# Kernel optimization log

Hardware: AMD Instinct MI355X
Metric: run time of the kernel (lower is better)

The kernel has to match this reference:

```python
import jax, jax.numpy as jnp
import numpy as np

CH = 64          # channels per plane
GS = 256         # base grid size
N_PTS = 500_000  # query points
BOUND = 1.0
A = -0.75        # torch bicubic coefficient


def _avg_pool(p):
    # torch F.avg_pool2d(kernel=3, stride=2, padding=1, count_include_pad=True) on (C,H,W)
    s = jax.lax.reduce_window(p, 0.0, jax.lax.add, (1, 3, 3), (1, 2, 2),
                              [(0, 0), (1, 1), (1, 1)])
    return s / 9.0


def _cubic_w(t):
    # Keys cubic conv weights (a=-0.75) for taps at offsets [-1,0,1,2]; t in [0,1). -> (4, M)
    def k1(x):  # |x| <= 1
        return ((A + 2.0) * x - (A + 3.0)) * x * x + 1.0
    def k2(x):  # 1 < |x| < 2
        return ((A * x - 5.0 * A) * x + 8.0 * A) * x - 4.0 * A
    return jnp.stack([k2(t + 1.0), k1(t), k1(1.0 - t), k2(2.0 - t)])


def _sample_plane(plane, gx, gy):
    # bicubic grid_sample, padding_mode='border', align_corners=True
    # plane: (C,H,W); gx,gy: (M,) grid coords in [-1,1] convention. -> (M,C)
    C, H, W = plane.shape
    x = (gx + 1.0) * 0.5 * (W - 1)  # unnormalize (align_corners=True)
    y = (gy + 1.0) * 0.5 * (H - 1)
    x0 = jnp.floor(x)
    y0 = jnp.floor(y)
    wx = _cubic_w(x - x0)  # (4,M)
    wy = _cubic_w(y - y0)  # (4,M)
    offs = jnp.arange(-1, 3, dtype=jnp.int32)[:, None]
    ix = jnp.clip(x0.astype(jnp.int32)[None, :] + offs, 0, W - 1)  # (4,M) border clamp
    iy = jnp.clip(y0.astype(jnp.int32)[None, :] + offs, 0, H - 1)
    out = jnp.zeros((C, x.shape[0]), plane.dtype)
    for j in range(4):
        row = wx[0] * plane[:, iy[j], ix[0]]
        for i in range(1, 4):
            row = row + wx[i] * plane[:, iy[j], ix[i]]  # (C,M) gather + fma
        out = out + wy[j] * row
    return out.T  # (M,C)


def setup_inputs() -> dict:
    key = jax.random.key(0)
    kc, kx, ky, kz = jax.random.split(key, 4)
    coordinates = jax.random.uniform(kc, (N_PTS, 3), jnp.float32, -1.0, 1.0)
    px0 = jax.random.normal(kx, (CH, GS, GS), jnp.float32) * 0.001
    py0 = jax.random.normal(ky, (CH, GS, GS), jnp.float32) * 0.001
    pz0 = jax.random.normal(kz, (CH, GS, GS), jnp.float32) * 0.001
    px1, py1, pz1 = _avg_pool(px0), _avg_pool(py0), _avg_pool(pz0)
    px2, py2, pz2 = _avg_pool(px1), _avg_pool(py1), _avg_pool(pz1)
    return dict(coordinates=coordinates, px0=px0, py0=py0, pz0=pz0,
                px1=px1, py1=py1, pz1=pz1, px2=px2, py2=py2, pz2=pz2)


def reference(coordinates, px0, py0, pz0, px1, py1, pz1, px2, py2, pz2):
    # Faithful to torch: coords mapped to [0,1] and fed to grid_sample as-is
    c = (coordinates + BOUND) / (2.0 * BOUND)  # (N,3), lives in [0,1] of the [-1,1] grid space
    feats = []
    for pxy, pyz, pxz in ((px0, py0, pz0), (px1, py1, pz1), (px2, py2, pz2)):
        f = (_sample_plane(pxy, c[:, 0], c[:, 1])
             + _sample_plane(pyz, c[:, 1], c[:, 2])
             + _sample_plane(pxz, c[:, 0], c[:, 2]))
        feats.append(f)
    return jnp.concatenate(feats, axis=-1)  # (N, 3*CH)
```

## Files before the change

### kernel.cpp

```cpp
#include <hip/hip_runtime.h>
#include <hip/hip_fp16.h>

#define NPTS 500000
#define NBINS 32768
#define NSUPER 8192
#define RSTRIDE 65

#define PLANE_SCALE 1024.0f
#define INV_PLANE_SCALE 0.0009765625f

__device__ __forceinline__ void cubic_w(float t, float w[4]) {
  const float a = -0.75f;
  const float t1 = t + 1.0f;
  w[0] = ((a * t1 - 5.0f * a) * t1 + 8.0f * a) * t1 - 4.0f * a;
  w[1] = ((a + 2.0f) * t - (a + 3.0f)) * t * t + 1.0f;
  const float u = 1.0f - t;
  w[2] = ((a + 2.0f) * u - (a + 3.0f)) * u * u + 1.0f;
  const float t2 = 2.0f - t;
  w[3] = ((a * t2 - 5.0f * a) * t2 + 8.0f * a) * t2 - 4.0f * a;
}

__global__ __launch_bounds__(256) void transpose_chw_hwc_f16(
    const float* __restrict__ p0, const float* __restrict__ p1,
    const float* __restrict__ p2, __half* __restrict__ dst, int HW) {
  __shared__ float lds[64][65];
  const float* src = (blockIdx.y == 0) ? p0 : ((blockIdx.y == 1) ? p1 : p2);
  __half* out = dst + (size_t)blockIdx.y * (size_t)HW * 64;
  const int pixBase = blockIdx.x * 64;
  const int tid = threadIdx.x;
  const int lane = tid & 63;
  const int quad = tid >> 6;
#pragma unroll
  for (int k = 0; k < 16; ++k) {
    const int c = k * 4 + quad;
    lds[c][lane] = src[(size_t)c * HW + pixBase + lane];
  }
  __syncthreads();
#pragma unroll
  for (int k = 0; k < 16; ++k) {
    const int pp = k * 4 + quad;
    out[(size_t)(pixBase + pp) * 64 + lane] =
        __float2half(lds[lane][pp] * PLANE_SCALE);
  }
}

__device__ __forceinline__ unsigned spread3(unsigned v) {
  return (v & 1u) | ((v & 2u) << 2) | ((v & 4u) << 4) | ((v & 8u) << 6) |
         ((v & 16u) << 8);
}

__device__ __forceinline__ unsigned compact3(unsigned v) {
  return (v & 1u) | ((v >> 2) & 2u) | ((v >> 4) & 4u) | ((v >> 6) & 8u) |
         ((v >> 8) & 16u);
}

__device__ __forceinline__ int bin_of(float cx, float cy, float cz) {
  int xq = (int)((cx + 1.0f) * 16.0f);
  int yq = (int)((cy + 1.0f) * 16.0f);
  int zq = (int)((cz + 1.0f) * 16.0f);
  xq = xq < 0 ? 0 : (xq > 31 ? 31 : xq);
  yq = yq < 0 ? 0 : (yq > 31 ? 31 : yq);
  zq = zq < 0 ? 0 : (zq > 31 ? 31 : zq);
  return (int)(spread3((unsigned)xq) | (spread3((unsigned)yq) << 1) |
               (spread3((unsigned)zq) << 2));
}

__global__ __launch_bounds__(256) void bin_count(
    const float* __restrict__ coords, int* __restrict__ counts) {
  const int pt = blockIdx.x * 256 + threadIdx.x;
  if (pt >= NPTS) return;
  const int b = bin_of(coords[pt * 3], coords[pt * 3 + 1], coords[pt * 3 + 2]);
  atomicAdd(&counts[b], 1);
}

__global__ __launch_bounds__(1024) void bin_scan(
    const int* __restrict__ counts, int* __restrict__ cursor) {
  __shared__ int lds[1024];
  const int t = threadIdx.x;
  const int base = t * 32;
  int s = 0;
#pragma unroll
  for (int i = 0; i < 32; ++i) s += counts[base + i];
  lds[t] = s;
  __syncthreads();
  int own = s;
  for (int off = 1; off < 1024; off <<= 1) {
    int v = (t >= off) ? lds[t - off] : 0;
    __syncthreads();
    lds[t] += v;
    __syncthreads();
  }
  int run = lds[t] - own;
#pragma unroll
  for (int i = 0; i < 32; ++i) {
    cursor[base + i] = run;
    run += counts[base + i];
  }
}

__global__ __launch_bounds__(256) void bin_scatter_prep(
    const float* __restrict__ coords, int* __restrict__ cursor,
    uint4* __restrict__ wrec) {
  const int pt = blockIdx.x * 256 + threadIdx.x;
  if (pt >= NPTS) return;
  const float x = coords[pt * 3], y = coords[pt * 3 + 1],
              z = coords[pt * 3 + 2];
  const int b = bin_of(x, y, z);
  const int pos = atomicAdd(&cursor[b], 1);

  const int qx0 = ((int)compact3((unsigned)b)) & ~1;
  const int qy0 = ((int)compact3((unsigned)b >> 1)) & ~1;
  const int qz = (int)compact3((unsigned)b >> 2);
  const float vin[3] = {x, y, z};

#pragma unroll
  for (int s = 0; s < 3; ++s) {
    const int W = (s == 0) ? 256 : ((s == 1) ? 128 : 64);
    const float hw = 0.5f * (float)(W - 1);
    const int fb[3] = {(int)floorf((1.0f + (float)qx0 * 0.03125f) * hw),
                       (int)floorf((1.0f + (float)qy0 * 0.03125f) * hw),
                       (int)floorf((1.0f + (float)qz * 0.03125f) * hw)};
    uint wp[6];
    int rel[3];
#pragma unroll
    for (int a = 0; a < 3; ++a) {
      const float c = (vin[a] + 1.0f) * 0.5f;
      const float gx = (c + 1.0f) * 0.5f * (float)(W - 1);
      const float x0f = floorf(gx);
      float w[4];
      cubic_w(gx - x0f, w);
      int r = (int)x0f - fb[a];
      const int rmax = (a == 2) ? 4 : 12;
      r = r < 0 ? 0 : (r > rmax ? rmax : r);
      rel[a] = r;
      const __half2 lo = __halves2half2(__float2half(w[0]), __float2half(w[1]));
      const __half2 hi = __halves2half2(__float2half(w[2]), __float2half(w[3]));
      wp[a * 2] = *(const uint*)&lo;
      wp[a * 2 + 1] = *(const uint*)&hi;
    }
    uint4* dst = wrec + ((size_t)s * NPTS + pos) * 2;
    dst[0] = make_uint4(wp[0], wp[1], wp[2], wp[3]);
    dst[1] = make_uint4(
        wp[4], wp[5],
        (uint)(rel[0] * 4) | ((uint)(rel[1] * 4) << 8) | ((uint)rel[2] << 16),
        (uint)pt);
  }
}

__global__ __launch_bounds__(256, 4) void sample_super(
    const uint4* __restrict__ wrec, const ushort* __restrict__ tp,
    const int* __restrict__ endc, float* __restrict__ out) {
  __shared__ uint4 win[32 * RSTRIDE];

  const int orig = blockIdx.x;
  const int sb = (orig & 7) * (NSUPER / 8) + (orig >> 3);
  const int b0 = sb * 4;
  const int start = (b0 == 0) ? 0 : endc[b0 - 1];
  const int end = endc[b0 + 3];
  if (start >= end) return;

  const int s = blockIdx.y;
  const int h = blockIdx.z;
  const int W = (s == 0) ? 256 : ((s == 1) ? 128 : 64);
  const size_t sbase = (s == 0) ? 0 : ((s == 1) ? 12582912 : 15728640);
  const size_t psz = (size_t)W * W * 64;
  const float hw = 0.5f * (float)(W - 1);

  const int qx0 = ((int)compact3((unsigned)b0)) & ~1;
  const int qy0 = ((int)compact3((unsigned)b0 >> 1)) & ~1;
  const int qz = (int)compact3((unsigned)b0 >> 2);
  const int wbx = (int)floorf((1.0f + (float)qx0 * 0.03125f) * hw) - 1;
  const int wby = (int)floorf((1.0f + (float)qy0 * 0.03125f) * hw) - 1;
  const int wbz = (int)floorf((1.0f + (float)qz * 0.03125f) * hw) - 1;

  const char* tpb = (const char*)(tp + sbase) + h * 64;
  const int tid = threadIdx.x;
  const int wave = tid >> 6;
  const int lane = tid & 63;
  const int px = lane >> 2;
  const int cgl = lane & 3;
#pragma unroll
  for (int k = 0; k < 8; ++k) {
    const int row = k * 4 + wave;
    int p, grow, cb;
    if (row < 16) {
      p = 0;
      grow = wby + row;
      cb = wbx;
    } else if (row < 24) {
      p = 1;
      grow = wbz + row - 16;
      cb = wby;
    } else {
      p = 2;
      grow = wbz + row - 24;
      cb = wbx;
    }
    grow = grow < 0 ? 0 : (grow > W - 1 ? W - 1 : grow);
    int gcol = cb + px;
    gcol = gcol < 0 ? 0 : (gcol > W - 1 ? W - 1 : gcol);
    const char* src = tpb + (size_t)p * psz * 2 +
                      ((size_t)grow * W + gcol) * 128 + cgl * 16;
#if __has_builtin(__builtin_amdgcn_global_load_lds)
    __builtin_amdgcn_global_load_lds((const uint*)src,
                                     (uint*)&win[row * RSTRIDE], 16, 0, 0);
#else
    win[row * RSTRIDE + lane] = *reinterpret_cast<const uint4*>(src);
#endif
  }
  __syncthreads();

  const int lanegrp = tid >> 2;
  const int cg = tid & 3;

  for (int i0 = start; i0 < end; i0 += 64) {
    const int slot = i0 + lanegrp;
    if (slot >= end) break;
    const uint4 r0 = wrec[((size_t)s * NPTS + slot) * 2];
    const uint4 r1 = wrec[((size_t)s * NPTS + slot) * 2 + 1];
    const int pt = (int)r1.w;
    const int relx4 = (int)(r1.z & 255u);
    const int rely4 = (int)((r1.z >> 8) & 255u);
    const int relz = (int)((r1.z >> 16) & 255u);
    const int rely = rely4 >> 2;

    const int xybase = rely * RSTRIDE + relx4 + cg;
    const int zrow = relz * RSTRIDE;
    const int yzbase = 16 * RSTRIDE + zrow + rely4 + cg;
    const int xzbase = 24 * RSTRIDE + zrow + relx4 + cg;

    __half2 wx[4], wy[4], wz[4];
    {
      const __half2 hx01 = *(const __half2*)&r0.x;
      const __half2 hx23 = *(const __half2*)&r0.y;
      const __half2 hy01 = *(const __half2*)&r0.z;
      const __half2 hy23 = *(const __half2*)&r0.w;
      const __half2 hz01 = *(const __half2*)&r1.x;
      const __half2 hz23 = *(const __half2*)&r1.y;
      wx[0] = __half2half2(__low2half(hx01));
      wx[1] = __half2half2(__high2half(hx01));
      wx[2] = __half2half2(__low2half(hx23));
      wx[3] = __half2half2(__high2half(hx23));
      wy[0] = __half2half2(__low2half(hy01));
      wy[1] = __half2half2(__high2half(hy01));
      wy[2] = __half2half2(__low2half(hy23));
      wy[3] = __half2half2(__high2half(hy23));
      wz[0] = __half2half2(__low2half(hz01));
      wz[1] = __half2half2(__high2half(hz01));
      wz[2] = __half2half2(__low2half(hz23));
      wz[3] = __half2half2(__high2half(hz23));
    }

    __half2 a0 = __float2half2_rn(0.0f), a1 = a0, a2 = a0, a3 = a0;

#define ROWTAPS(BASEPTR, CW, RW_j)                                    \
  {                                                                   \
    const uint4* bp = (BASEPTR);                                      \
    __half2 q0 = __float2half2_rn(0.0f), q1 = q0, q2 = q0, q3 = q0;   \
    _Pragma("unroll") for (int i = 0; i < 4; ++i) {                   \
      const uint4 v = bp[4 * i];                                      \
      q0 = __hfma2(CW[i], *(const __half2*)&v.x, q0);                 \
      q1 = __hfma2(CW[i], *(const __half2*)&v.y, q1);                 \
      q2 = __hfma2(CW[i], *(const __half2*)&v.z, q2);                 \
      q3 = __hfma2(CW[i], *(const __half2*)&v.w, q3);                 \
    }                                                                 \
    a0 = __hfma2(RW_j, q0, a0);                                       \
    a1 = __hfma2(RW_j, q1, a1);                                       \
    a2 = __hfma2(RW_j, q2, a2);                                       \
    a3 = __hfma2(RW_j, q3, a3);                                       \
  }

#pragma unroll
    for (int j = 0; j < 4; ++j)
      ROWTAPS(&win[xybase + j * RSTRIDE], wx, wy[j]);
#pragma unroll
    for (int j = 0; j < 4; ++j)
      ROWTAPS(&win[yzbase + j * RSTRIDE], wy, wz[j]);
#pragma unroll
    for (int j = 0; j < 4; ++j)
      ROWTAPS(&win[xzbase + j * RSTRIDE], wx, wz[j]);
#undef ROWTAPS

    const float2 f0 = __half22float2(a0);
    const float2 f1 = __half22float2(a1);
    const float2 f2 = __half22float2(a2);
    const float2 f3 = __half22float2(a3);
    float* optr = out + (size_t)pt * 192 + s * 64 + h * 32 + cg * 8;
    *reinterpret_cast<float4*>(optr) =
        make_float4(f0.x * INV_PLANE_SCALE, f0.y * INV_PLANE_SCALE,
                    f1.x * INV_PLANE_SCALE, f1.y * INV_PLANE_SCALE);
    *reinterpret_cast<float4*>(optr + 4) =
        make_float4(f2.x * INV_PLANE_SCALE, f2.y * INV_PLANE_SCALE,
                    f3.x * INV_PLANE_SCALE, f3.y * INV_PLANE_SCALE);
  }
}

__device__ __forceinline__ void sample_acc_chw(const float* __restrict__ plane,
                                               int W, float gx, float gy,
                                               int cg, float4& acc) {
  const float x = (gx + 1.0f) * 0.5f * (float)(W - 1);
  const float y = (gy + 1.0f) * 0.5f * (float)(W - 1);
  const float x0f = floorf(x), y0f = floorf(y);
  float wx[4], wy[4];
  cubic_w(x - x0f, wx);
  cubic_w(y - y0f, wy);
  const int x0 = (int)x0f, y0 = (int)y0f;
  int ix[4], iy[4];
#pragma unroll
  for (int i = 0; i < 4; ++i) {
    int xi = x0 - 1 + i;
    ix[i] = xi < 0 ? 0 : (xi > W - 1 ? W - 1 : xi);
    int yi = y0 - 1 + i;
    iy[i] = yi < 0 ? 0 : (yi > W - 1 ? W - 1 : yi);
  }
  const size_t HW = (size_t)W * W;
  float r[4] = {acc.x, acc.y, acc.z, acc.w};
#pragma unroll
  for (int cc = 0; cc < 4; ++cc) {
    const float* pc = plane + (size_t)(cg * 4 + cc) * HW;
    float a = 0.f;
#pragma unroll
    for (int j = 0; j < 4; ++j) {
      const float* rb = pc + (size_t)iy[j] * W;
      float row = 0.f;
#pragma unroll
      for (int i = 0; i < 4; ++i) row += wx[i] * rb[ix[i]];
      a += wy[j] * row;
    }
    r[cc] += a;
  }
  acc = make_float4(r[0], r[1], r[2], r[3]);
}

__global__ __launch_bounds__(256) void sample_fallback(
    const float* __restrict__ coords, const float* __restrict__ px0,
    const float* __restrict__ py0, const float* __restrict__ pz0,
    const float* __restrict__ px1, const float* __restrict__ py1,
    const float* __restrict__ pz1, const float* __restrict__ px2,
    const float* __restrict__ py2, const float* __restrict__ pz2,
    float* __restrict__ out) {
  const int t = blockIdx.x * 256 + threadIdx.x;
  const int pt = t >> 4;
  const int cg = t & 15;
  if (pt >= NPTS) return;
  const float cx = (coords[pt * 3 + 0] + 1.0f) * 0.5f;
  const float cy = (coords[pt * 3 + 1] + 1.0f) * 0.5f;
  const float cz = (coords[pt * 3 + 2] + 1.0f) * 0.5f;
  const float* xs[3] = {px0, px1, px2};
  const float* ys[3] = {py0, py1, py2};
  const float* zs[3] = {pz0, pz1, pz2};
  const int sw[3] = {256, 128, 64};
  float* optr = out + (size_t)pt * 192 + cg * 4;
#pragma unroll
  for (int s = 0; s < 3; ++s) {
    const int W = sw[s];
    float4 acc = make_float4(0.f, 0.f, 0.f, 0.f);
    sample_acc_chw(xs[s], W, cx, cy, cg, acc);
    sample_acc_chw(ys[s], W, cy, cz, cg, acc);
    sample_acc_chw(zs[s], W, cx, cz, cg, acc);
    *reinterpret_cast<float4*>(optr + s * 64) = acc;
  }
}

extern "C" void kernel_launch(void* const* d_in, const int* in_sizes, int n_in,
                              void* d_out, int out_size, void* d_ws,
                              size_t ws_size, hipStream_t stream) {
  const float* coords = (const float*)d_in[0];
  const float* px0 = (const float*)d_in[1];
  const float* py0 = (const float*)d_in[2];
  const float* pz0 = (const float*)d_in[3];
  const float* px1 = (const float*)d_in[4];
  const float* py1 = (const float*)d_in[5];
  const float* pz1 = (const float*)d_in[6];
  const float* px2 = (const float*)d_in[7];
  const float* py2 = (const float*)d_in[8];
  const float* pz2 = (const float*)d_in[9];
  float* out = (float*)d_out;

  const size_t TP_BYTES = 33030144;
  const size_t CNT_OFF = TP_BYTES;
  const size_t CUR_OFF = CNT_OFF + 131072;
  const size_t REC_OFF = CUR_OFF + 131072;
  const size_t NEEDED = REC_OFF + (size_t)NPTS * 3 * 32;

  if (ws_size >= NEEDED) {
    __half* tp = (__half*)d_ws;
    int* counts = (int*)((char*)d_ws + CNT_OFF);
    int* cursor = (int*)((char*)d_ws + CUR_OFF);
    uint4* wrec = (uint4*)((char*)d_ws + REC_OFF);

    transpose_chw_hwc_f16<<<dim3(65536 / 64, 3), 256, 0, stream>>>(
        px0, py0, pz0, tp + 0, 65536);
    transpose_chw_hwc_f16<<<dim3(16384 / 64, 3), 256, 0, stream>>>(
        px1, py1, pz1, tp + 12582912, 16384);
    transpose_chw_hwc_f16<<<dim3(4096 / 64, 3), 256, 0, stream>>>(
        px2, py2, pz2, tp + 15728640, 4096);

    hipMemsetAsync(counts, 0, NBINS * sizeof(int), stream);
    const int pblocks = (NPTS + 255) / 256;
    bin_count<<<pblocks, 256, 0, stream>>>(coords, counts);
    bin_scan<<<1, 1024, 0, stream>>>(counts, cursor);
    bin_scatter_prep<<<pblocks, 256, 0, stream>>>(coords, cursor, wrec);

    sample_super<<<dim3(NSUPER, 3, 2), 256, 0, stream>>>(
        wrec, (const ushort*)tp, cursor, out);
  } else {
    const int sample_blocks = (NPTS * 16 + 255) / 256;
    sample_fallback<<<sample_blocks, 256, 0, stream>>>(
        coords, px0, py0, pz0, px1, py1, pz1, px2, py2, pz2, out);
  }
}
```

Before: 320.5 us.

## Split each point's taps across lane pairs with shuffle reduction and unpadded LDS

Each point is now handled by 8 lanes instead of 4. Each lane pair splits the four horizontal taps into two column pairs, premultiplies the row and column weights, and combines its partials with an xor shuffle before each lane writes half of the output channels. The LDS window loses its 65-stride padding and moves to a flat 64 stride. The goal is to shorten the per-point dependency chain and raise parallelism per block. The cost is twice as many loop iterations per block, extra shuffles, and possible LDS bank conflicts now that the padding is gone.

```diff
diff --git a/kernel.cpp b/kernel.cpp
--- a/kernel.cpp
+++ b/kernel.cpp
@@ -4,7 +4,6 @@
 #define NPTS 500000
 #define NBINS 32768
 #define NSUPER 8192
-#define RSTRIDE 65
 
 #define PLANE_SCALE 1024.0f
 #define INV_PLANE_SCALE 0.0009765625f
@@ -150,7 +149,7 @@
 __global__ __launch_bounds__(256, 4) void sample_super(
     const uint4* __restrict__ wrec, const ushort* __restrict__ tp,
     const int* __restrict__ endc, float* __restrict__ out) {
-  __shared__ uint4 win[32 * RSTRIDE];
+  __shared__ uint4 win[2048];
 
   const int orig = blockIdx.x;
   const int sb = (orig & 7) * (NSUPER / 8) + (orig >> 3);
@@ -203,17 +202,19 @@
                       ((size_t)grow * W + gcol) * 128 + cgl * 16;
 #if __has_builtin(__builtin_amdgcn_global_load_lds)
     __builtin_amdgcn_global_load_lds((const uint*)src,
-                                     (uint*)&win[row * RSTRIDE], 16, 0, 0);
+                                     (uint*)&win[row * 64], 16, 0, 0);
 #else
-    win[row * RSTRIDE + lane] = *reinterpret_cast<const uint4*>(src);
+    win[row * 64 + lane] = *reinterpret_cast<const uint4*>(src);
 #endif
   }
   __syncthreads();
 
-  const int lanegrp = tid >> 2;
+  const int lanegrp = tid >> 3;
   const int cg = tid & 3;
-
-  for (int i0 = start; i0 < end; i0 += 64) {
+  const int colpair = (tid >> 2) & 1;
+  const int c8 = colpair * 8 + cg;
+
+  for (int i0 = start; i0 < end; i0 += 32) {
     const int slot = i0 + lanegrp;
     if (slot >= end) break;
     const uint4 r0 = wrec[((size_t)s * NPTS + slot) * 2];
@@ -224,74 +225,77 @@
     const int relz = (int)((r1.z >> 16) & 255u);
     const int rely = rely4 >> 2;
 
-    const int xybase = rely * RSTRIDE + relx4 + cg;
-    const int zrow = relz * RSTRIDE;
-    const int yzbase = 16 * RSTRIDE + zrow + rely4 + cg;
-    const int xzbase = 24 * RSTRIDE + zrow + relx4 + cg;
-
-    __half2 wx[4], wy[4], wz[4];
+    const __half2 hx01 = *(const __half2*)&r0.x;
+    const __half2 hx23 = *(const __half2*)&r0.y;
+    const __half2 hy01 = *(const __half2*)&r0.z;
+    const __half2 hy23 = *(const __half2*)&r0.w;
+    const __half2 hz01 = *(const __half2*)&r1.x;
+    const __half2 hz23 = *(const __half2*)&r1.y;
+    __half2 wyb[4], wzb[4];
+    wyb[0] = __half2half2(__low2half(hy01));
+    wyb[1] = __half2half2(__high2half(hy01));
+    wyb[2] = __half2half2(__low2half(hy23));
+    wyb[3] = __half2half2(__high2half(hy23));
+    wzb[0] = __half2half2(__low2half(hz01));
+    wzb[1] = __half2half2(__high2half(hz01));
+    wzb[2] = __half2half2(__low2half(hz23));
+    wzb[3] = __half2half2(__high2half(hz23));
+    const __half2 hxsel = colpair ? hx23 : hx01;
+    const __half2 hysel = colpair ? hy23 : hy01;
+    const __half2 cxA = __half2half2(__low2half(hxsel));
+    const __half2 cxB = __half2half2(__high2half(hxsel));
+    const __half2 cyA = __half2half2(__low2half(hysel));
+    const __half2 cyB = __half2half2(__high2half(hysel));
+
+    const int bXY = rely * 64 + relx4 + c8;
+    const int bYZ = 1024 + relz * 64 + rely4 + c8;
+    const int bXZ = 1536 + relz * 64 + relx4 + c8;
+
+    __half2 acc0 = __float2half2_rn(0.0f), acc1 = acc0, acc2 = acc0,
+            acc3 = acc0;
+
+#define PLANE(BASE, CWA, CWB, RW)                                   \
+  _Pragma("unroll") for (int j = 0; j < 4; ++j) {                   \
+    const __half2 mA = __hmul2(CWA, RW[j]);                         \
+    const __half2 mB = __hmul2(CWB, RW[j]);                         \
+    const uint4 vA = win[(BASE) + j * 64];                          \
+    const uint4 vB = win[(BASE) + j * 64 + 4];                      \
+    acc0 = __hfma2(mA, *(const __half2*)&vA.x, acc0);               \
+    acc1 = __hfma2(mA, *(const __half2*)&vA.y, acc1);               \
+    acc2 = __hfma2(mA, *(const __half2*)&vA.z, acc2);               \
+    acc3 = __hfma2(mA, *(const __half2*)&vA.w, acc3);               \
+    acc0 = __hfma2(mB, *(const __half2*)&vB.x, acc0);               \
+    acc1 = __hfma2(mB, *(const __half2*)&vB.y, acc1);               \
+    acc2 = __hfma2(mB, *(const __half2*)&vB.z, acc2);               \
+    acc3 = __hfma2(mB, *(const __half2*)&vB.w, acc3);               \
+  }
+
+    PLANE(bXY, cxA, cxB, wyb);
+    PLANE(bYZ, cyA, cyB, wzb);
+    PLANE(bXZ, cxA, cxB, wzb);
+#undef PLANE
+
     {
-      const __half2 hx01 = *(const __half2*)&r0.x;
-      const __half2 hx23 = *(const __half2*)&r0.y;
-      const __half2 hy01 = *(const __half2*)&r0.z;
-      const __half2 hy23 = *(const __half2*)&r0.w;
-      const __half2 hz01 = *(const __half2*)&r1.x;
-      const __half2 hz23 = *(const __half2*)&r1.y;
-      wx[0] = __half2half2(__low2half(hx01));
-      wx[1] = __half2half2(__high2half(hx01));
-      wx[2] = __half2half2(__low2half(hx23));
-      wx[3] = __half2half2(__high2half(hx23));
-      wy[0] = __half2half2(__low2half(hy01));
-      wy[1] = __half2half2(__high2half(hy01));
-      wy[2] = __half2half2(__low2half(hy23));
-      wy[3] = __half2half2(__high2half(hy23));
-      wz[0] = __half2half2(__low2half(hz01));
-      wz[1] = __half2half2(__high2half(hz01));
-      wz[2] = __half2half2(__low2half(hz23));
-      wz[3] = __half2half2(__high2half(hz23));
+      uint u0 = *(const uint*)&acc0, u1 = *(const uint*)&acc1,
+           u2 = *(const uint*)&acc2, u3 = *(const uint*)&acc3;
+      const uint p0 = __shfl_xor((int)u0, 4, 64);
+      const uint p1 = __shfl_xor((int)u1, 4, 64);
+      const uint p2 = __shfl_xor((int)u2, 4, 64);
+      const uint p3 = __shfl_xor((int)u3, 4, 64);
+      acc0 = __hadd2(acc0, *(const __half2*)&p0);
+      acc1 = __hadd2(acc1, *(const __half2*)&p1);
+      acc2 = __hadd2(acc2, *(const __half2*)&p2);
+      acc3 = __hadd2(acc3, *(const __half2*)&p3);
     }
 
-    __half2 a0 = __float2half2_rn(0.0f), a1 = a0, a2 = a0, a3 = a0;
-
-#define ROWTAPS(BASEPTR, CW, RW_j)                                    \
-  {                                                                   \
-    const uint4* bp = (BASEPTR);                                      \
-    __half2 q0 = __float2half2_rn(0.0f), q1 = q0, q2 = q0, q3 = q0;   \
-    _Pragma("unroll") for (int i = 0; i < 4; ++i) {                   \
-      const uint4 v = bp[4 * i];                                      \
-      q0 = __hfma2(CW[i], *(const __half2*)&v.x, q0);                 \
-      q1 = __hfma2(CW[i], *(const __half2*)&v.y, q1);                 \
-      q2 = __hfma2(CW[i], *(const __half2*)&v.z, q2);                 \
-      q3 = __hfma2(CW[i], *(const __half2*)&v.w, q3);                 \
-    }                                                                 \
-    a0 = __hfma2(RW_j, q0, a0);                                       \
-    a1 = __hfma2(RW_j, q1, a1);                                       \
-    a2 = __hfma2(RW_j, q2, a2);                                       \
-    a3 = __hfma2(RW_j, q3, a3);                                       \
-  }
-
-#pragma unroll
-    for (int j = 0; j < 4; ++j)
-      ROWTAPS(&win[xybase + j * RSTRIDE], wx, wy[j]);
-#pragma unroll
-    for (int j = 0; j < 4; ++j)
-      ROWTAPS(&win[yzbase + j * RSTRIDE], wy, wz[j]);
-#pragma unroll
-    for (int j = 0; j < 4; ++j)
-      ROWTAPS(&win[xzbase + j * RSTRIDE], wx, wz[j]);
-#undef ROWTAPS
-
-    const float2 f0 = __half22float2(a0);
-    const float2 f1 = __half22float2(a1);
-    const float2 f2 = __half22float2(a2);
-    const float2 f3 = __half22float2(a3);
-    float* optr = out + (size_t)pt * 192 + s * 64 + h * 32 + cg * 8;
-    *reinterpret_cast<float4*>(optr) =
+    const __half2 o0 = colpair ? acc2 : acc0;
+    const __half2 o1 = colpair ? acc3 : acc1;
+    const float2 f0 = __half22float2(o0);
+    const float2 f1 = __half22float2(o1);
+    *reinterpret_cast<float4*>(out + (size_t)pt * 192 + s * 64 + h * 32 +
+                               cg * 8 + colpair * 4) =
         make_float4(f0.x * INV_PLANE_SCALE, f0.y * INV_PLANE_SCALE,
                     f1.x * INV_PLANE_SCALE, f1.y * INV_PLANE_SCALE);
-    *reinterpret_cast<float4*>(optr + 4) =
-        make_float4(f2.x * INV_PLANE_SCALE, f2.y * INV_PLANE_SCALE,
-                    f3.x * INV_PLANE_SCALE, f3.y * INV_PLANE_SCALE);
   }
 }
 
```

After: 320.8 us. Within noise of the previous version (+0.1%).
